# Optimization experiments

Hardware: AMD Instinct MI355X
Metric: run time of the kernel (lower is better)

The kernel has to match this reference:

```python
import jax, jax.numpy as jnp
import numpy as np

B, S, C = 4, 2048, 1024
DK = C // 4   # 256, q/k projection dim
DO = 1024     # out_channels


def setup_inputs() -> dict:
    key = jax.random.key(0)
    ks = jax.random.split(key, 7)
    s = 1.0 / np.sqrt(C)
    return {
        "x": jax.random.normal(ks[0], (B, S, C), dtype=jnp.float32),
        "Wq": jax.random.uniform(ks[1], (C, DK), jnp.float32, -s, s),
        "bq": jax.random.uniform(ks[2], (DK,), jnp.float32, -s, s),
        "Wk": jax.random.uniform(ks[3], (C, DK), jnp.float32, -s, s),
        "bk": jax.random.uniform(ks[4], (DK,), jnp.float32, -s, s),
        "Wv": jax.random.uniform(ks[5], (C, DO), jnp.float32, -s, s),
        "bv": jax.random.uniform(ks[6], (DO,), jnp.float32, -s, s),
    }


def reference(x, Wq, bq, Wk, bk, Wv, bv):
    q = jnp.einsum("bsc,cd->bsd", x, Wq) + bq   # [B,S,DK]
    k = jnp.einsum("bsc,cd->bsd", x, Wk) + bk   # [B,S,DK]
    v = jnp.einsum("bsc,cd->bsd", x, Wv) + bv   # [B,S,DO]
    scores = jnp.einsum("bqd,bkd->bqk", q, k) / jnp.sqrt(jnp.float32(DK))
    attn = jax.nn.softmax(scores, axis=-1)      # [B,S,S]
    return jnp.einsum("bqk,bkd->bqd", attn, v)  # [B,S,DO]
```

## Files before the change

### kernel.cpp

```cpp
#include <hip/hip_runtime.h>
#include <hip/hip_bf16.h>

typedef __attribute__((ext_vector_type(8))) short short8;
typedef __attribute__((ext_vector_type(8))) __bf16 bf16x8;
typedef __attribute__((ext_vector_type(4))) float f32x4;

#define MFMA(a, b, c) __builtin_amdgcn_mfma_f32_16x16x32_bf16((a), (b), (c), 0, 0, 0)
#define SCALE 0.0625f

static __device__ __forceinline__ void gload16(const void* g, void* l) {
  __builtin_amdgcn_global_load_lds(
      (const __attribute__((address_space(1))) void*)g,
      (__attribute__((address_space(3))) void*)l, 16, 0, 0);
}

static __device__ __forceinline__ unsigned short f2b(float f) {
  union { __hip_bfloat16 h; unsigned short u; } cv;
  cv.h = __float2bfloat16(f);
  return cv.u;
}

__global__ __launch_bounds__(256) void convert_x_kern(const float* __restrict__ x,
                                                      unsigned short* __restrict__ xb) {
  long i = ((long)blockIdx.x * 256 + threadIdx.x) * 8;
  float4 a = *reinterpret_cast<const float4*>(x + i);
  float4 b = *reinterpret_cast<const float4*>(x + i + 4);
  short8 o;
  o[0] = (short)f2b(a.x); o[1] = (short)f2b(a.y); o[2] = (short)f2b(a.z); o[3] = (short)f2b(a.w);
  o[4] = (short)f2b(b.x); o[5] = (short)f2b(b.y); o[6] = (short)f2b(b.z); o[7] = (short)f2b(b.w);
  *reinterpret_cast<short8*>(xb + i) = o;
}

__global__ void pack_bias_kern(const float* __restrict__ bq, const float* __restrict__ bk,
                               const float* __restrict__ bv, float* __restrict__ bc) {
  int i = blockIdx.x * 256 + threadIdx.x;
  float v = (i < 256) ? bq[i] : (i < 512) ? bk[i - 256] : bv[i - 512];
  bc[i] = v;
}

__global__ __launch_bounds__(256) void transpose_w_kern(const float* __restrict__ src,
                                                        unsigned short* __restrict__ dst,
                                                        int ldsrc, int lddst) {
  __shared__ __align__(16) unsigned short tile[64][72];
  int r0 = blockIdx.y * 64, c0 = blockIdx.x * 64;
  int t = threadIdx.x;
  #pragma unroll
  for (int it = 0; it < 4; ++it) {
    int idx = it * 1024 + t * 4;
    int row = idx >> 6, col = idx & 63;
    float4 v = *reinterpret_cast<const float4*>(src + (long)(r0 + row) * ldsrc + c0 + col);
    tile[row][col + 0] = f2b(v.x); tile[row][col + 1] = f2b(v.y);
    tile[row][col + 2] = f2b(v.z); tile[row][col + 3] = f2b(v.w);
  }
  __syncthreads();
  #pragma unroll
  for (int it = 0; it < 4; ++it) {
    int idx = it * 1024 + t * 4;
    int orow = idx >> 6, ocol = idx & 63;
    ushort4 o;
    o.x = tile[ocol + 0][orow]; o.y = tile[ocol + 1][orow];
    o.z = tile[ocol + 2][orow]; o.w = tile[ocol + 3][orow];
    *reinterpret_cast<ushort4*>(dst + (long)(c0 + orow) * lddst + r0 + ocol) = o;
  }
}

__global__ __launch_bounds__(256) void transpose_v_kern(const unsigned short* __restrict__ src0,
                                                        unsigned short* __restrict__ dst0,
                                                        int ldsrc, int lddst,
                                                        long sbatch, long dbatch) {
  const unsigned short* src = src0 + (long)blockIdx.z * sbatch;
  unsigned short* dst = dst0 + (long)blockIdx.z * dbatch;
  __shared__ __align__(16) unsigned short tile[64][72];
  int r0 = blockIdx.y * 64, c0 = blockIdx.x * 64;
  int t = threadIdx.x;
  #pragma unroll
  for (int it = 0; it < 2; ++it) {
    int idx = it * 2048 + t * 8;
    int row = idx >> 6, col = idx & 63;
    short8 v = *reinterpret_cast<const short8*>(src + (long)(r0 + row) * ldsrc + c0 + col);
    *reinterpret_cast<short8*>(&tile[row][col]) = v;
  }
  __syncthreads();
  #pragma unroll
  for (int it = 0; it < 2; ++it) {
    int idx = it * 2048 + t * 8;
    int orow = idx >> 6, ocol = idx & 63;
    short8 o;
    #pragma unroll
    for (int i = 0; i < 8; ++i) o[i] = (short)tile[ocol + i][orow];
    *reinterpret_cast<short8*>(dst + (long)(c0 + orow) * lddst + r0 + ocol) = o;
  }
}

template <int BM, int SWZ, bool BF16OUT, bool BIAS, bool RS, bool EXPSUM>
__global__ __launch_bounds__(512, 2) void gemm_pi(
    const unsigned short* __restrict__ A, const unsigned short* __restrict__ B,
    const float* __restrict__ bias, void* __restrict__ Cout,
    int NT, int lda, int ldb, int ldc,
    long batchA, long batchB, long batchC,
    const float* __restrict__ rowscale,
    float* __restrict__ lpart) {
  constexpr int WM = BM / 2;
  constexpr int ASH = BM * 64;
  constexpr int TSH = ASH + 256 * 64;
  __shared__ __align__(128) unsigned short lds[2 * TSH];

  int bid = blockIdx.x;
  int b = 0, tm, tn;
  if constexpr (SWZ == 0) {
    int xcd = bid & 7, s = bid >> 3;
    tm = xcd * 4 + s / 6; tn = s % 6;
  } else {
    int xcd = bid & 7, s = bid >> 3;
    b = xcd >> 1; tm = (xcd & 1) * 4 + (s >> 3); tn = s & 7;
  }

  int t = threadIdx.x, w = t >> 6, l = t & 63;
  int wr = w >> 2, wc = w & 3;
  int g = l >> 4, c = l & 15;

  f32x4 acc[WM / 16][4];
  #pragma unroll
  for (int m = 0; m < WM / 16; ++m)
    #pragma unroll
    for (int n = 0; n < 4; ++n) acc[m][n] = (f32x4){0.f, 0.f, 0.f, 0.f};

  int srow = t >> 3;
  int scb = (t & 7) * 16;
  const unsigned short* aptr = A + (long)b * batchA + (long)(tm * BM) * lda;
  const unsigned short* bptr = B + (long)b * batchB + (long)(tn * 256) * ldb;
  int kb = scb ^ ((srow & 7) << 4);

  auto stageA = [&](int buf, int k0, int r) {
    int row = r * 64 + srow;
    gload16(aptr + (long)row * lda + k0 + (kb >> 1),
            lds + buf * TSH + r * 4096 + t * 8);
  };
  auto stageB = [&](int buf, int k0, int r) {
    int row = r * 64 + srow;
    gload16(bptr + (long)row * ldb + k0 + (kb >> 1),
            lds + buf * TSH + ASH + r * 4096 + t * 8);
  };
  auto ldA = [&](const char* abase, int mh, int kh, int m) {
    int row = wr * WM + mh * 64 + m * 16 + c;
    int pb = row * 128 + (kh * 32 + g * 8) * 2;
    pb ^= ((pb >> 7) & 7) << 4;
    return *reinterpret_cast<const bf16x8*>(abase + pb);
  };
  auto ldB = [&](const char* bbase, int kh, int n) {
    int row = wc * 64 + n * 16 + c;
    int pb = row * 128 + (kh * 32 + g * 8) * 2;
    pb ^= ((pb >> 7) & 7) << 4;
    return *reinterpret_cast<const bf16x8*>(bbase + pb);
  };

  stageB(0, 0, 0); stageB(0, 0, 1); stageB(0, 0, 2); stageB(0, 0, 3);
  stageA(0, 0, 0); stageA(0, 0, 2); stageA(0, 0, 1); stageA(0, 0, 3);
  asm volatile("s_waitcnt vmcnt(0)" ::: "memory");
  __builtin_amdgcn_s_barrier();

  for (int kt = 0; kt < NT; ++kt) {
    int cur = kt & 1, nb = cur ^ 1;
    const char* abase = (const char*)(lds + cur * TSH);
    const char* bbase = (const char*)(lds + cur * TSH + ASH);
    bool more = (kt + 1) < NT;
    int k1 = (kt + 1) * 64;
    bf16x8 bfr[4];
    #pragma unroll
    for (int p = 0; p < 4; ++p) {
      const int kh = p >> 1, mh = p & 1;
      bf16x8 af[4];
      #pragma unroll
      for (int m = 0; m < 4; ++m) af[m] = ldA(abase, mh, kh, m);
      if (mh == 0) {
        #pragma unroll
        for (int n = 0; n < 4; ++n) bfr[n] = ldB(bbase, kh, n);
      }
      if (more) {
        if      (p == 0) { stageB(nb, k1, 0); stageB(nb, k1, 1); }
        else if (p == 1) { stageB(nb, k1, 2); stageB(nb, k1, 3); }
        else if (p == 2) { stageA(nb, k1, 0); stageA(nb, k1, 2); }
        else             { stageA(nb, k1, 1); stageA(nb, k1, 3); }
      }
      __builtin_amdgcn_s_barrier();
      asm volatile("s_waitcnt lgkmcnt(0)" ::: "memory");
      __builtin_amdgcn_sched_barrier(0);
      __builtin_amdgcn_s_setprio(1);
      #pragma unroll
      for (int m = 0; m < 4; ++m)
        #pragma unroll
        for (int n = 0; n < 4; ++n)
          acc[mh * 4 + m][n] = MFMA(af[m], bfr[n], acc[mh * 4 + m][n]);
      __builtin_amdgcn_s_setprio(0);
      if (p == 0) {
        if (kt == NT - 1) asm volatile("s_waitcnt vmcnt(0)" ::: "memory");
        else              asm volatile("s_waitcnt vmcnt(2)" ::: "memory");
      }
      if (p == 3 && more) {
        asm volatile("s_waitcnt vmcnt(2)" ::: "memory");
      }
      __builtin_amdgcn_s_barrier();
    }
  }

  int rbase = tm * BM + wr * WM + g * 4;
  int c0 = tn * 256 + wc * 64 + c;

  if constexpr (EXPSUM) {
    __shared__ float lred[4][BM];
    #pragma unroll
    for (int mi = 0; mi < WM / 16; ++mi) {
      int roff = (mi / 4) * 64 + (mi % 4) * 16;
      #pragma unroll
      for (int j = 0; j < 4; ++j) {
        long ob = (long)b * batchC + (long)(rbase + roff + j) * ldc + c0;
        float rs = 0.f;
        #pragma unroll
        for (int n = 0; n < 4; ++n) {
          float pv = __expf(acc[mi][n][j] * SCALE);
          ((unsigned short*)Cout)[ob + n * 16] = f2b(pv);
          rs += pv;
        }
        rs += __shfl_xor(rs, 1); rs += __shfl_xor(rs, 2);
        rs += __shfl_xor(rs, 4); rs += __shfl_xor(rs, 8);
        if (c == 0) lred[wc][wr * WM + roff + g * 4 + j] = rs;
      }
    }
    __syncthreads();
    for (int rr = t; rr < BM; rr += 512) {
      float s = lred[0][rr] + lred[1][rr] + lred[2][rr] + lred[3][rr];
      lpart[((long)b * 2048 + tm * BM + rr) * 8 + tn] = s;
    }
  } else {
    #pragma unroll
    for (int mi = 0; mi < WM / 16; ++mi) {
      int roff = (mi / 4) * 64 + (mi % 4) * 16;
      float lv[4];
      if (RS) {
        #pragma unroll
        for (int j = 0; j < 4; ++j)
          lv[j] = rowscale[(long)b * 2048 + rbase + roff + j];
      }
      #pragma unroll
      for (int n = 0; n < 4; ++n) {
        int col = c0 + n * 16;
        float bv = BIAS ? bias[col] : 0.f;
        long rowb = (long)b * batchC + (long)(rbase + roff) * ldc + col;
        #pragma unroll
        for (int j = 0; j < 4; ++j) {
          float v = acc[mi][n][j] + bv;
          if (RS) v *= lv[j];
          if (BF16OUT) ((unsigned short*)Cout)[rowb + (long)j * ldc] = f2b(v);
          else         ((float*)Cout)[rowb + (long)j * ldc] = v;
        }
      }
    }
  }
}

__global__ __launch_bounds__(512, 2) void gemm_pp(
    const unsigned short* __restrict__ A, const unsigned short* __restrict__ B,
    float* __restrict__ Cout,
    int NT, int lda, int ldb, int ldc,
    long batchA, long batchB, long batchC,
    const float* __restrict__ rowscale) {
  constexpr int ASH = 128 * 64;
  constexpr int TSH = ASH + 256 * 64;
  __shared__ __align__(128) unsigned short lds[3 * TSH];

  int bid = blockIdx.x;
  int xcd = bid & 7, s = bid >> 3;
  int b = xcd >> 1;
  int tm = (xcd & 1) * 8 + (s >> 2), tn = s & 3;

  int t = threadIdx.x, w = t >> 6, l = t & 63;
  int wr = w >> 2, wc = w & 3;
  int g = l >> 4, c = l & 15;

  f32x4 acc[4][4];
  #pragma unroll
  for (int m = 0; m < 4; ++m)
    #pragma unroll
    for (int n = 0; n < 4; ++n) acc[m][n] = (f32x4){0.f, 0.f, 0.f, 0.f};

  int srow = t >> 3;
  int scb = (t & 7) * 16;
  int kb = scb ^ ((srow & 7) << 4);
  const unsigned short* aptr = A + (long)b * batchA + (long)(tm * 128) * lda;
  const unsigned short* bptr = B + (long)b * batchB + (long)(tn * 256) * ldb;

  auto stage6 = [&](int buf, int kt2) {
    int k0 = kt2 * 64;
    #pragma unroll
    for (int r = 0; r < 4; ++r) {
      int row = r * 64 + srow;
      gload16(bptr + (long)row * ldb + k0 + (kb >> 1),
              lds + buf * TSH + ASH + r * 4096 + t * 8);
    }
    #pragma unroll
    for (int r = 0; r < 2; ++r) {
      int row = r * 64 + srow;
      gload16(aptr + (long)row * lda + k0 + (kb >> 1),
              lds + buf * TSH + r * 4096 + t * 8);
    }
  };

  stage6(0, 0); stage6(1, 1);
  asm volatile("s_waitcnt vmcnt(6)" ::: "memory");
  __builtin_amdgcn_s_barrier();
  if (wr == 1) __builtin_amdgcn_s_barrier();

  for (int hs = 0; hs < 2 * NT; ++hs) {
    int kt = hs >> 1, kh = hs & 1;
    const char* abase = (const char*)(lds + (kt % 3) * TSH);
    const char* bbase = abase + ASH * 2;

    bf16x8 af[4], bfr[4];
    #pragma unroll
    for (int m = 0; m < 4; ++m) {
      int row = wr * 64 + m * 16 + c;
      int pb = row * 128 + (kh * 32 + g * 8) * 2;
      pb ^= ((pb >> 7) & 7) << 4;
      af[m] = *reinterpret_cast<const bf16x8*>(abase + pb);
    }
    #pragma unroll
    for (int n = 0; n < 4; ++n) {
      int row = wc * 64 + n * 16 + c;
      int pb = row * 128 + (kh * 32 + g * 8) * 2;
      pb ^= ((pb >> 7) & 7) << 4;
      bfr[n] = *reinterpret_cast<const bf16x8*>(bbase + pb);
    }

    if (kh == 1) {
      if (kt + 2 < NT) stage6((kt + 2) % 3, kt + 2);
      if (wr == 1) {
        if (kt < NT - 2)       asm volatile("s_waitcnt vmcnt(6)" ::: "memory");
        else if (kt == NT - 2) asm volatile("s_waitcnt vmcnt(0)" ::: "memory");
      }
    }
    __builtin_amdgcn_s_barrier();
    asm volatile("s_waitcnt lgkmcnt(0)" ::: "memory");
    __builtin_amdgcn_sched_barrier(0);
    __builtin_amdgcn_s_setprio(1);
    #pragma unroll
    for (int m = 0; m < 4; ++m)
      #pragma unroll
      for (int n = 0; n < 4; ++n)
        acc[m][n] = MFMA(af[m], bfr[n], acc[m][n]);
    __builtin_amdgcn_s_setprio(0);
    if (kh == 1 && wr == 0) {
      if (kt < NT - 2)       asm volatile("s_waitcnt vmcnt(6)" ::: "memory");
      else if (kt == NT - 2) asm volatile("s_waitcnt vmcnt(0)" ::: "memory");
    }
    __builtin_amdgcn_s_barrier();
  }
  if (wr == 0) __builtin_amdgcn_s_barrier();

  int rbase = tm * 128 + wr * 64 + g * 4;
  int c0 = tn * 256 + wc * 64 + c;
  #pragma unroll
  for (int mi = 0; mi < 4; ++mi) {
    int roff = mi * 16;
    float lv[4];
    #pragma unroll
    for (int j = 0; j < 4; ++j)
      lv[j] = rowscale[(long)b * 2048 + rbase + roff + j];
    #pragma unroll
    for (int n = 0; n < 4; ++n) {
      int col = c0 + n * 16;
      long rowb = (long)b * batchC + (long)(rbase + roff) * ldc + col;
      #pragma unroll
      for (int j = 0; j < 4; ++j)
        Cout[rowb + (long)j * ldc] = acc[mi][n][j] * lv[j];
    }
  }
}

__global__ __launch_bounds__(256) void linv_kern(const float* __restrict__ lpart,
                                                 float* __restrict__ linv) {
  int r = blockIdx.x * 256 + threadIdx.x;
  float s = 0.f;
  #pragma unroll
  for (int i = 0; i < 8; ++i) s += lpart[(long)r * 8 + i];
  linv[r] = 1.f / s;
}

extern "C" void kernel_launch(void* const* d_in, const int* in_sizes, int n_in,
                              void* d_out, int out_size, void* d_ws, size_t ws_size,
                              hipStream_t stream) {
  (void)in_sizes; (void)n_in; (void)out_size; (void)ws_size;
  const float* x  = (const float*)d_in[0];
  const float* Wq = (const float*)d_in[1];
  const float* bq = (const float*)d_in[2];
  const float* Wk = (const float*)d_in[3];
  const float* bk = (const float*)d_in[4];
  const float* Wv = (const float*)d_in[5];
  const float* bv = (const float*)d_in[6];
  float* out = (float*)d_out;
  char* ws = (char*)d_ws;

  unsigned short* xb   = (unsigned short*)(ws + 0);
  float*          lpart= (float*)         (ws + 0);
  float*          linv = (float*)         (ws + 262144);
  unsigned short* wt   = (unsigned short*)(ws + 16777216);
  float*          bc   = (float*)         (ws + 19922944);
  unsigned short* qkv  = (unsigned short*)(ws + 19929088);
  unsigned short* vT   = (unsigned short*)(ws + 45094912);
  unsigned short* attn = (unsigned short*)(ws + 61872128);

  convert_x_kern<<<4096, 256, 0, stream>>>(x, xb);
  pack_bias_kern<<<6, 256, 0, stream>>>(bq, bk, bv, bc);
  transpose_w_kern<<<dim3(4, 16), 256, 0, stream>>>(Wq, wt,              256, 1024);
  transpose_w_kern<<<dim3(4, 16), 256, 0, stream>>>(Wk, wt + 256 * 1024, 256, 1024);
  transpose_w_kern<<<dim3(16, 16), 256, 0, stream>>>(Wv, wt + 512 * 1024, 1024, 1024);

  gemm_pi<256, 0, true, true, false, false><<<dim3(192), 512, 0, stream>>>(
      xb, wt, bc, qkv, 16, 1024, 1024, 1536, 0, 0, 0, nullptr, nullptr);

  transpose_v_kern<<<dim3(16, 32, 4), 256, 0, stream>>>(
      qkv + 512, vT, 1536, 2048, (long)2048 * 1536, (long)1024 * 2048);

  gemm_pi<256, 1, true, false, false, true><<<dim3(256), 512, 0, stream>>>(
      qkv, qkv + 256, nullptr, attn, 4, 1536, 1536, 2048,
      (long)2048 * 1536, (long)2048 * 1536, (long)2048 * 2048, nullptr, lpart);
  linv_kern<<<32, 256, 0, stream>>>(lpart, linv);

  gemm_pp<<<dim3(256), 512, 0, stream>>>(
      attn, vT, out, 32, 2048, 2048, 1024,
      (long)2048 * 2048, (long)1024 * 2048, (long)2048 * 1024, linv);
}
```

Before: 123.0 us.

## Fuse V transpose into QKV GEMM epilogue and simplify PV pipeline

The QKV projection GEMM now writes the V tiles directly in transposed layout from its epilogue, removing the separate transpose kernel and its extra read and write of V. The attention-times-V GEMM is rewritten to process a full 64-wide k step per iteration with a single barrier instead of staggered half-step barriers across wave rows. The transposed stores are 8-byte scattered writes, and the new pipeline schedule changes how memory and MFMA work overlap.

```diff
diff --git a/kernel.cpp b/kernel.cpp
--- a/kernel.cpp
+++ b/kernel.cpp
@@ -64,44 +64,16 @@
   }
 }
 
-__global__ __launch_bounds__(256) void transpose_v_kern(const unsigned short* __restrict__ src0,
-                                                        unsigned short* __restrict__ dst0,
-                                                        int ldsrc, int lddst,
-                                                        long sbatch, long dbatch) {
-  const unsigned short* src = src0 + (long)blockIdx.z * sbatch;
-  unsigned short* dst = dst0 + (long)blockIdx.z * dbatch;
-  __shared__ __align__(16) unsigned short tile[64][72];
-  int r0 = blockIdx.y * 64, c0 = blockIdx.x * 64;
-  int t = threadIdx.x;
-  #pragma unroll
-  for (int it = 0; it < 2; ++it) {
-    int idx = it * 2048 + t * 8;
-    int row = idx >> 6, col = idx & 63;
-    short8 v = *reinterpret_cast<const short8*>(src + (long)(r0 + row) * ldsrc + c0 + col);
-    *reinterpret_cast<short8*>(&tile[row][col]) = v;
-  }
-  __syncthreads();
-  #pragma unroll
-  for (int it = 0; it < 2; ++it) {
-    int idx = it * 2048 + t * 8;
-    int orow = idx >> 6, ocol = idx & 63;
-    short8 o;
-    #pragma unroll
-    for (int i = 0; i < 8; ++i) o[i] = (short)tile[ocol + i][orow];
-    *reinterpret_cast<short8*>(dst + (long)(c0 + orow) * lddst + r0 + ocol) = o;
-  }
-}
-
-template <int BM, int SWZ, bool BF16OUT, bool BIAS, bool RS, bool EXPSUM>
+template <int SWZ, bool BIAS, bool VSPLIT, bool EXPSUM>
 __global__ __launch_bounds__(512, 2) void gemm_pi(
     const unsigned short* __restrict__ A, const unsigned short* __restrict__ B,
     const float* __restrict__ bias, void* __restrict__ Cout,
     int NT, int lda, int ldb, int ldc,
     long batchA, long batchB, long batchC,
-    const float* __restrict__ rowscale,
-    float* __restrict__ lpart) {
-  constexpr int WM = BM / 2;
-  constexpr int ASH = BM * 64;
+    float* __restrict__ lpart,
+    unsigned short* __restrict__ vT) {
+  constexpr int WM = 128;
+  constexpr int ASH = 256 * 64;
   constexpr int TSH = ASH + 256 * 64;
   __shared__ __align__(128) unsigned short lds[2 * TSH];
 
@@ -119,15 +91,15 @@
   int wr = w >> 2, wc = w & 3;
   int g = l >> 4, c = l & 15;
 
-  f32x4 acc[WM / 16][4];
-  #pragma unroll
-  for (int m = 0; m < WM / 16; ++m)
+  f32x4 acc[8][4];
+  #pragma unroll
+  for (int m = 0; m < 8; ++m)
     #pragma unroll
     for (int n = 0; n < 4; ++n) acc[m][n] = (f32x4){0.f, 0.f, 0.f, 0.f};
 
   int srow = t >> 3;
   int scb = (t & 7) * 16;
-  const unsigned short* aptr = A + (long)b * batchA + (long)(tm * BM) * lda;
+  const unsigned short* aptr = A + (long)b * batchA + (long)(tm * 256) * lda;
   const unsigned short* bptr = B + (long)b * batchB + (long)(tn * 256) * ldb;
   int kb = scb ^ ((srow & 7) << 4);
 
@@ -203,13 +175,13 @@
     }
   }
 
-  int rbase = tm * BM + wr * WM + g * 4;
+  int rbase = tm * 256 + wr * WM + g * 4;
   int c0 = tn * 256 + wc * 64 + c;
 
   if constexpr (EXPSUM) {
-    __shared__ float lred[4][BM];
-    #pragma unroll
-    for (int mi = 0; mi < WM / 16; ++mi) {
+    __shared__ float lred[4][256];
+    #pragma unroll
+    for (int mi = 0; mi < 8; ++mi) {
       int roff = (mi / 4) * 64 + (mi % 4) * 16;
       #pragma unroll
       for (int j = 0; j < 4; ++j) {
@@ -227,51 +199,58 @@
       }
     }
     __syncthreads();
-    for (int rr = t; rr < BM; rr += 512) {
+    for (int rr = t; rr < 256; rr += 512) {
       float s = lred[0][rr] + lred[1][rr] + lred[2][rr] + lred[3][rr];
-      lpart[((long)b * 2048 + tm * BM + rr) * 8 + tn] = s;
+      lpart[((long)b * 2048 + tm * 256 + rr) * 8 + tn] = s;
+    }
+  } else if (VSPLIT && tn >= 2) {
+    int bb = tm >> 3;
+    #pragma unroll
+    for (int mi = 0; mi < 8; ++mi) {
+      int roff = (mi / 4) * 64 + (mi % 4) * 16;
+      int s0 = (rbase + roff) & 2047;
+      #pragma unroll
+      for (int n = 0; n < 4; ++n) {
+        int col = c0 + n * 16;
+        float bv = BIAS ? bias[col] : 0.f;
+        ushort4 pk;
+        pk.x = f2b(acc[mi][n][0] + bv); pk.y = f2b(acc[mi][n][1] + bv);
+        pk.z = f2b(acc[mi][n][2] + bv); pk.w = f2b(acc[mi][n][3] + bv);
+        *reinterpret_cast<ushort4*>(vT + (long)bb * 2097152 +
+                                    (long)(col - 512) * 2048 + s0) = pk;
+      }
     }
   } else {
     #pragma unroll
-    for (int mi = 0; mi < WM / 16; ++mi) {
+    for (int mi = 0; mi < 8; ++mi) {
       int roff = (mi / 4) * 64 + (mi % 4) * 16;
-      float lv[4];
-      if (RS) {
-        #pragma unroll
-        for (int j = 0; j < 4; ++j)
-          lv[j] = rowscale[(long)b * 2048 + rbase + roff + j];
-      }
       #pragma unroll
       for (int n = 0; n < 4; ++n) {
         int col = c0 + n * 16;
         float bv = BIAS ? bias[col] : 0.f;
         long rowb = (long)b * batchC + (long)(rbase + roff) * ldc + col;
         #pragma unroll
-        for (int j = 0; j < 4; ++j) {
-          float v = acc[mi][n][j] + bv;
-          if (RS) v *= lv[j];
-          if (BF16OUT) ((unsigned short*)Cout)[rowb + (long)j * ldc] = f2b(v);
-          else         ((float*)Cout)[rowb + (long)j * ldc] = v;
-        }
-      }
-    }
-  }
-}
-
-__global__ __launch_bounds__(512, 2) void gemm_pp(
-    const unsigned short* __restrict__ A, const unsigned short* __restrict__ B,
+        for (int j = 0; j < 4; ++j)
+          ((unsigned short*)Cout)[rowb + (long)j * ldc] = f2b(acc[mi][n][j] + bv);
+      }
+    }
+  }
+}
+
+__global__ __launch_bounds__(512, 2) void gemm_pv(
+    const unsigned short* __restrict__ A,
+    const unsigned short* __restrict__ B,
     float* __restrict__ Cout,
-    int NT, int lda, int ldb, int ldc,
-    long batchA, long batchB, long batchC,
-    const float* __restrict__ rowscale) {
+    const float* __restrict__ linv) {
+  constexpr int NT = 32;
   constexpr int ASH = 128 * 64;
   constexpr int TSH = ASH + 256 * 64;
   __shared__ __align__(128) unsigned short lds[3 * TSH];
 
   int bid = blockIdx.x;
-  int xcd = bid & 7, s = bid >> 3;
+  int xcd = bid & 7, sidx = bid >> 3;
   int b = xcd >> 1;
-  int tm = (xcd & 1) * 8 + (s >> 2), tn = s & 3;
+  int tm = (xcd & 1) * 8 + (sidx >> 2), tn = sidx & 3;
 
   int t = threadIdx.x, w = t >> 6, l = t & 63;
   int wr = w >> 2, wc = w & 3;
@@ -286,92 +265,89 @@
   int srow = t >> 3;
   int scb = (t & 7) * 16;
   int kb = scb ^ ((srow & 7) << 4);
-  const unsigned short* aptr = A + (long)b * batchA + (long)(tm * 128) * lda;
-  const unsigned short* bptr = B + (long)b * batchB + (long)(tn * 256) * ldb;
-
-  auto stage6 = [&](int buf, int kt2) {
-    int k0 = kt2 * 64;
+  const unsigned short* aptr = A + (long)b * 4194304 + (long)(tm * 128) * 2048;
+  const unsigned short* bptr = B + (long)b * 2097152 + (long)(tn * 256) * 2048;
+
+  auto stageA = [&](int buf, int k0) {
+    #pragma unroll
+    for (int r = 0; r < 2; ++r) {
+      int row = r * 64 + srow;
+      gload16(aptr + (long)row * 2048 + k0 + (kb >> 1),
+              lds + buf * TSH + r * 4096 + t * 8);
+    }
+  };
+  auto stageB = [&](int buf, int k0) {
     #pragma unroll
     for (int r = 0; r < 4; ++r) {
       int row = r * 64 + srow;
-      gload16(bptr + (long)row * ldb + k0 + (kb >> 1),
+      gload16(bptr + (long)row * 2048 + k0 + (kb >> 1),
               lds + buf * TSH + ASH + r * 4096 + t * 8);
     }
-    #pragma unroll
-    for (int r = 0; r < 2; ++r) {
-      int row = r * 64 + srow;
-      gload16(aptr + (long)row * lda + k0 + (kb >> 1),
-              lds + buf * TSH + r * 4096 + t * 8);
-    }
-  };
-
-  stage6(0, 0); stage6(1, 1);
+  };
+
+  stageA(0, 0); stageB(0, 0);
+  stageA(1, 64); stageB(1, 64);
   asm volatile("s_waitcnt vmcnt(6)" ::: "memory");
   __builtin_amdgcn_s_barrier();
-  if (wr == 1) __builtin_amdgcn_s_barrier();
-
-  for (int hs = 0; hs < 2 * NT; ++hs) {
-    int kt = hs >> 1, kh = hs & 1;
-    const char* abase = (const char*)(lds + (kt % 3) * TSH);
+
+  for (int kt = 0; kt < NT; ++kt) {
+    int cur = kt % 3, nxt = (kt + 2) % 3;
+    const char* abase = (const char*)(lds + cur * TSH);
     const char* bbase = abase + ASH * 2;
 
-    bf16x8 af[4], bfr[4];
-    #pragma unroll
-    for (int m = 0; m < 4; ++m) {
-      int row = wr * 64 + m * 16 + c;
-      int pb = row * 128 + (kh * 32 + g * 8) * 2;
-      pb ^= ((pb >> 7) & 7) << 4;
-      af[m] = *reinterpret_cast<const bf16x8*>(abase + pb);
-    }
-    #pragma unroll
-    for (int n = 0; n < 4; ++n) {
-      int row = wc * 64 + n * 16 + c;
-      int pb = row * 128 + (kh * 32 + g * 8) * 2;
-      pb ^= ((pb >> 7) & 7) << 4;
-      bfr[n] = *reinterpret_cast<const bf16x8*>(bbase + pb);
-    }
-
-    if (kh == 1) {
-      if (kt + 2 < NT) stage6((kt + 2) % 3, kt + 2);
-      if (wr == 1) {
-        if (kt < NT - 2)       asm volatile("s_waitcnt vmcnt(6)" ::: "memory");
-        else if (kt == NT - 2) asm volatile("s_waitcnt vmcnt(0)" ::: "memory");
-      }
-    }
-    __builtin_amdgcn_s_barrier();
-    asm volatile("s_waitcnt lgkmcnt(0)" ::: "memory");
-    __builtin_amdgcn_sched_barrier(0);
+    bf16x8 af[2][4], bf[2][4];
+    #pragma unroll
+    for (int sk = 0; sk < 2; ++sk) {
+      #pragma unroll
+      for (int m = 0; m < 4; ++m) {
+        int p = (wr * 64 + m * 16 + c) * 128 + (sk * 32 + g * 8) * 2;
+        p ^= ((p >> 7) & 7) << 4;
+        af[sk][m] = *reinterpret_cast<const bf16x8*>(abase + p);
+      }
+      #pragma unroll
+      for (int n = 0; n < 4; ++n) {
+        int p = (wc * 64 + n * 16 + c) * 128 + (sk * 32 + g * 8) * 2;
+        p ^= ((p >> 7) & 7) << 4;
+        bf[sk][n] = *reinterpret_cast<const bf16x8*>(bbase + p);
+      }
+    }
+
+    if (kt + 2 < NT) {
+      int k2 = (kt + 2) * 64;
+      stageA(nxt, k2); stageB(nxt, k2);
+    }
+
     __builtin_amdgcn_s_setprio(1);
     #pragma unroll
-    for (int m = 0; m < 4; ++m)
-      #pragma unroll
-      for (int n = 0; n < 4; ++n)
-        acc[m][n] = MFMA(af[m], bfr[n], acc[m][n]);
+    for (int sk = 0; sk < 2; ++sk)
+      #pragma unroll
+      for (int m = 0; m < 4; ++m)
+        #pragma unroll
+        for (int n = 0; n < 4; ++n)
+          acc[m][n] = MFMA(af[sk][m], bf[sk][n], acc[m][n]);
     __builtin_amdgcn_s_setprio(0);
-    if (kh == 1 && wr == 0) {
-      if (kt < NT - 2)       asm volatile("s_waitcnt vmcnt(6)" ::: "memory");
-      else if (kt == NT - 2) asm volatile("s_waitcnt vmcnt(0)" ::: "memory");
-    }
-    __builtin_amdgcn_s_barrier();
-  }
-  if (wr == 0) __builtin_amdgcn_s_barrier();
+
+    if (kt < NT - 1) {
+      if (kt == NT - 2) asm volatile("s_waitcnt vmcnt(0)" ::: "memory");
+      else              asm volatile("s_waitcnt vmcnt(6)" ::: "memory");
+      __builtin_amdgcn_s_barrier();
+    }
+  }
 
   int rbase = tm * 128 + wr * 64 + g * 4;
   int c0 = tn * 256 + wc * 64 + c;
   #pragma unroll
   for (int mi = 0; mi < 4; ++mi) {
-    int roff = mi * 16;
     float lv[4];
     #pragma unroll
     for (int j = 0; j < 4; ++j)
-      lv[j] = rowscale[(long)b * 2048 + rbase + roff + j];
+      lv[j] = linv[(long)b * 2048 + rbase + mi * 16 + j];
     #pragma unroll
     for (int n = 0; n < 4; ++n) {
-      int col = c0 + n * 16;
-      long rowb = (long)b * batchC + (long)(rbase + roff) * ldc + col;
+      long rowb = (long)b * 2097152 + (long)(rbase + mi * 16) * 1024 + c0 + n * 16;
       #pragma unroll
       for (int j = 0; j < 4; ++j)
-        Cout[rowb + (long)j * ldc] = acc[mi][n][j] * lv[j];
+        Cout[rowb + (long)j * 1024] = acc[mi][n][j] * lv[j];
     }
   }
 }
@@ -414,18 +390,13 @@
   transpose_w_kern<<<dim3(4, 16), 256, 0, stream>>>(Wk, wt + 256 * 1024, 256, 1024);
   transpose_w_kern<<<dim3(16, 16), 256, 0, stream>>>(Wv, wt + 512 * 1024, 1024, 1024);
 
-  gemm_pi<256, 0, true, true, false, false><<<dim3(192), 512, 0, stream>>>(
-      xb, wt, bc, qkv, 16, 1024, 1024, 1536, 0, 0, 0, nullptr, nullptr);
-
-  transpose_v_kern<<<dim3(16, 32, 4), 256, 0, stream>>>(
-      qkv + 512, vT, 1536, 2048, (long)2048 * 1536, (long)1024 * 2048);
-
-  gemm_pi<256, 1, true, false, false, true><<<dim3(256), 512, 0, stream>>>(
+  gemm_pi<0, true, true, false><<<dim3(192), 512, 0, stream>>>(
+      xb, wt, bc, qkv, 16, 1024, 1024, 1536, 0, 0, 0, nullptr, vT);
+
+  gemm_pi<1, false, false, true><<<dim3(256), 512, 0, stream>>>(
       qkv, qkv + 256, nullptr, attn, 4, 1536, 1536, 2048,
-      (long)2048 * 1536, (long)2048 * 1536, (long)2048 * 2048, nullptr, lpart);
+      (long)2048 * 1536, (long)2048 * 1536, (long)2048 * 2048, lpart, nullptr);
   linv_kern<<<32, 256, 0, stream>>>(lpart, linv);
 
-  gemm_pp<<<dim3(256), 512, 0, stream>>>(
-      attn, vT, out, 32, 2048, 2048, 1024,
-      (long)2048 * 2048, (long)1024 * 2048, (long)2048 * 1024, linv);
-}
+  gemm_pv<<<dim3(256), 512, 0, stream>>>(attn, vT, out, linv);
+}
```

New measurement: 114.9 us. 6.5% less time.
